# Kernel optimization log

Measured on AMD Instinct MI355X. Metric: run time of the kernel, lower is better.

## Reference

```python
import jax, jax.numpy as jnp
import numpy as np

N_NODES = 50000
N_EDGES = 600000
F_IN = 128
H = 128
NUM_GRAPHS = 64
SELF_LOOP_W = 2.0  # improved=True


def setup_inputs() -> dict:
    key = jax.random.key(0)
    ks = jax.random.split(key, 16)
    x = jax.random.normal(ks[0], (N_NODES, F_IN), dtype=jnp.float32)
    edge_index = jax.random.randint(ks[1], (2, N_EDGES), 0, N_NODES, dtype=jnp.int64)
    batch_index = jnp.sort(jax.random.randint(ks[2], (N_NODES,), 0, NUM_GRAPHS, dtype=jnp.int64))
    edge_weight = jax.random.uniform(ks[3], (N_EDGES,), dtype=jnp.float32)
    def lin(k, fin, fout):
        s = 1.0 / np.sqrt(fin)
        kw, kb = jax.random.split(k)
        W = jax.random.uniform(kw, (fin, fout), minval=-s, maxval=s, dtype=jnp.float32)
        b = jax.random.uniform(kb, (fout,), minval=-s, maxval=s, dtype=jnp.float32)
        return W, b
    W0, b0 = lin(ks[4], F_IN, H)
    W1, b1 = lin(ks[5], H, H)
    W2, b2 = lin(ks[6], H, H)
    W3, b3 = lin(ks[7], H, H)
    Wout, bout = lin(ks[8], 2 * H, 1)
    return dict(x=x, edge_index=edge_index, batch_index=batch_index, edge_weight=edge_weight,
                W0=W0, b0=b0, W1=W1, b1=b1, W2=W2, b2=b2, W3=W3, b3=b3, Wout=Wout, bout=bout)


def reference(x, edge_index, batch_index, edge_weight, W0, b0, W1, b1, W2, b2, W3, b3, Wout, bout):
    N = x.shape[0]
    loop = jnp.arange(N)
    src = jnp.concatenate([edge_index[0], loop])  # [E+N]
    dst = jnp.concatenate([edge_index[1], loop])
    w = jnp.concatenate([edge_weight, jnp.full((N,), SELF_LOOP_W, dtype=x.dtype)])
    # symmetric GCN normalization: deg over destination, norm = d^-1/2[src]*w*d^-1/2[dst]
    deg = jax.ops.segment_sum(w, dst, num_segments=N)
    dinv = jnp.where(deg > 0, jax.lax.rsqrt(deg), 0.0)
    norm = dinv[src] * w * dinv[dst]  # [E+N]

    def conv(h, W, b):
        h = h @ W  # dense transform before aggregation
        msg = h[src] * norm[:, None]
        return jax.ops.segment_sum(msg, dst, num_segments=N) + b

    h = jnp.tanh(conv(x, W0, b0))
    h = jnp.tanh(conv(h, W1, b1))
    h = jnp.tanh(conv(h, W2, b2))
    h = jnp.tanh(conv(h, W3, b3))

    gmax = jax.ops.segment_max(h, batch_index, num_segments=NUM_GRAPHS)
    gmax = jnp.where(jnp.isfinite(gmax), gmax, 0.0)  # guard empty graphs
    cnt = jax.ops.segment_sum(jnp.ones((N,), dtype=h.dtype), batch_index, num_segments=NUM_GRAPHS)
    gmean = jax.ops.segment_sum(h, batch_index, num_segments=NUM_GRAPHS) / jnp.maximum(cnt, 1.0)[:, None]
    hidden = jnp.concatenate([gmax, gmean], axis=1)  # [B, 2H]
    out = hidden @ Wout + bout  # [B, 1]
    return out, hidden
```

## Files before the change

kernel.cpp:

```cpp
#include <hip/hip_runtime.h>
#include <hip/hip_bf16.h>
#include <hip/hip_fp16.h>

typedef __hip_bfloat16 bf16;
typedef _Float16 half8 __attribute__((ext_vector_type(8)));
typedef float f32x4 __attribute__((ext_vector_type(4)));

#define FDIM 128
#define SELF_W 2.0f
#define NGRAPH 64
#define DEG_SCALE 1048576.0f
#define DEG_MASK  ((1ull<<44) - 1ull)

__device__ __forceinline__ float b2f(bf16 v){ return __bfloat162float(v); }

__device__ __forceinline__ float rdf(const void* p, long long i, int f32){
  return f32 ? ((const float*)p)[i] : b2f(((const bf16*)p)[i]);
}
__device__ __forceinline__ int rdi(const void* p, long long i, int i64){
  return i64 ? (int)(((const long long*)p)[i]) : ((const int*)p)[i];
}

__device__ __forceinline__ float tanh_fast(float x){
  float ax = fabsf(x);
  float e  = __expf(-2.0f*ax);
  float r  = (1.0f - e) * __builtin_amdgcn_rcpf(1.0f + e);
  return copysignf(r, x);
}

__global__ __launch_bounds__(256) void k_probe(const unsigned short* __restrict__ x16,
                                               const int* __restrict__ ei32,
                                               int* __restrict__ flags){
  __shared__ int cbig, codd;
  int tid = threadIdx.x;
  if (tid == 0){ cbig = 0; codd = 0; }
  __syncthreads();
  for (int i = tid; i < 4096; i += 256){
    int e = (x16[i] >> 7) & 0xFF;
    if (e >= 134) atomicAdd(&cbig, 1);
  }
  for (int i = tid; i < 512; i += 256){
    if (ei32[2*i + 1] != 0) atomicAdd(&codd, 1);
  }
  __syncthreads();
  if (tid == 0){
    flags[0] = (cbig >= 64) ? 1 : 0;
    flags[1] = (codd < 8)  ? 1 : 0;
  }
}

struct PtrPack { const void* p[10]; };
__global__ __launch_bounds__(256) void k_setup(PtrPack pk, float* __restrict__ pf,
                                               _Float16* __restrict__ wt,
                                               unsigned long long* __restrict__ packed,
                                               const void* __restrict__ bat,
                                               unsigned* __restrict__ gstart,
                                               int N, const int* __restrict__ flags){
  const int sz[10]  = {16384,16384,16384,16384,128,128,128,128,256,1};
  const int dst[10] = {0,16384,32768,49152,65536,65664,65792,65920,66048,66304};
  int i = blockIdx.x*blockDim.x + threadIdx.x;
  if (i < 66305){
    int seg = 0, rem = i;
    while (rem >= sz[seg]){ rem -= sz[seg]; seg++; }
    float v = rdf(pk.p[seg], rem, flags[0]);
    pf[dst[seg] + rem] = v;
    if (seg < 4){
      int k = rem >> 7, n = rem & 127;
      wt[seg*16384 + n*128 + k] = (_Float16)v;
    }
  }
  int stride = gridDim.x*blockDim.x;
  for (int j = i; j < N; j += stride)
    packed[j] = (unsigned long long)(SELF_W * DEG_SCALE);
  if (blockIdx.x == gridDim.x - 1){
    __shared__ unsigned s[NGRAPH+1];
    int g = threadIdx.x;
    int i64 = flags[1];
    if (g <= NGRAPH){
      int lo = 0, hi = N;
      while (lo < hi){ int mid = (lo + hi) >> 1; if (rdi(bat, mid, i64) < g) lo = mid + 1; else hi = mid; }
      s[g] = (unsigned)lo;
    }
    __syncthreads();
    if (g <= NGRAPH) gstart[g] = s[g];
  }
}

__global__ void k_edge_deg(const void* __restrict__ ei, const void* __restrict__ ew,
                           unsigned long long* __restrict__ packed,
                           unsigned* __restrict__ rank,
                           int E, int N, const int* __restrict__ flags){
  int e = blockIdx.x*blockDim.x + threadIdx.x;
  if (e >= E) return;
  int d = rdi(ei, (long long)E + e, flags[1]);
  unsigned r = 0u;
  if ((unsigned)d < (unsigned)N){
    float w = rdf(ew, e, flags[0]);
    unsigned long long add = (1ull << 44) |
        (unsigned long long)__float2uint_rn(w * DEG_SCALE);
    unsigned long long old = atomicAdd(&packed[d], add);
    r = (unsigned)(old >> 44);
  }
  rank[e] = r;
}

__device__ __forceinline__ unsigned wave_incl_scan(unsigned v){
  int lane = threadIdx.x & 63;
  #pragma unroll
  for (int d = 1; d < 64; d <<= 1){
    unsigned t = __shfl_up(v, d, 64);
    if (lane >= d) v += t;
  }
  return v;
}

__global__ __launch_bounds__(256) void k_scan_pre(const unsigned long long* __restrict__ packed,
                                                  float* __restrict__ dinv,
                                                  float* __restrict__ swv,
                                                  unsigned* __restrict__ bsum,
                                                  unsigned* __restrict__ epk, unsigned Epad,
                                                  int N){
  __shared__ unsigned wsh[4];
  int tid = threadIdx.x, lane = tid & 63, wid = tid >> 6;
  unsigned gid = blockIdx.x*blockDim.x + tid, gstr = gridDim.x*blockDim.x;
  for (unsigned j = gid; j < Epad; j += gstr) epk[j] = 0u;
  int i0 = blockIdx.x*1024 + tid*4;
  unsigned tsum = 0u;
  #pragma unroll
  for (int j = 0; j < 4; j++){
    int i = i0 + j;
    if (i < N){
      unsigned long long pv = packed[i];
      tsum += ((unsigned)(pv >> 44) + 7u) & ~7u;
      float d = (float)(pv & DEG_MASK) * (1.0f / DEG_SCALE);
      float di = (d > 0.f) ? rsqrtf(d) : 0.f;
      dinv[i] = di;
      swv[i]  = di * di * SELF_W;
    }
  }
  #pragma unroll
  for (int d = 1; d < 64; d <<= 1) tsum += __shfl_down(tsum, d, 64);
  if (lane == 0) wsh[wid] = tsum;
  __syncthreads();
  if (tid == 0) bsum[blockIdx.x] = wsh[0] + wsh[1] + wsh[2] + wsh[3];
}

__global__ __launch_bounds__(64) void k_scan_mid(unsigned* __restrict__ bsum,
                                                 unsigned* __restrict__ off,
                                                 int nb, int N){
  int lane = threadIdx.x;
  unsigned v = (lane < nb) ? bsum[lane] : 0u;
  unsigned isc = wave_incl_scan(v);
  if (lane < nb) bsum[lane] = isc - v;
  if (lane == 63) off[N] = isc;
}

__global__ __launch_bounds__(256) void k_scan_fin(const unsigned long long* __restrict__ packed,
                                                  const unsigned* __restrict__ bsum,
                                                  unsigned* __restrict__ off, int N){
  __shared__ unsigned wsh[4];
  int tid = threadIdx.x, lane = tid & 63, wid = tid >> 6;
  int i0 = blockIdx.x*1024 + tid*4;
  unsigned v0=0u,v1=0u,v2=0u,v3=0u;
  if (i0+0 < N) v0 = ((unsigned)(packed[i0+0] >> 44) + 7u) & ~7u;
  if (i0+1 < N) v1 = ((unsigned)(packed[i0+1] >> 44) + 7u) & ~7u;
  if (i0+2 < N) v2 = ((unsigned)(packed[i0+2] >> 44) + 7u) & ~7u;
  if (i0+3 < N) v3 = ((unsigned)(packed[i0+3] >> 44) + 7u) & ~7u;
  unsigned tsum = v0+v1+v2+v3;
  unsigned isc = wave_incl_scan(tsum);
  if (lane == 63) wsh[wid] = isc;
  __syncthreads();
  unsigned wbase = 0u;
  #pragma unroll
  for (int w = 0; w < 4; w++) if (w < wid) wbase += wsh[w];
  unsigned ex = bsum[blockIdx.x] + wbase + (isc - tsum);
  if (i0+0 < N) off[i0+0] = ex;
  if (i0+1 < N) off[i0+1] = ex + v0;
  if (i0+2 < N) off[i0+2] = ex + v0 + v1;
  if (i0+3 < N) off[i0+3] = ex + v0 + v1 + v2;
}

__global__ void k_bucket(const void* __restrict__ ei, const void* __restrict__ ew,
                         const float* __restrict__ dinv,
                         const unsigned* __restrict__ off,
                         const unsigned* __restrict__ rank,
                         unsigned* __restrict__ epk,
                         int E, unsigned Epad, int N, const int* __restrict__ flags){
  int e = blockIdx.x*blockDim.x + threadIdx.x;
  if (e >= E) return;
  int s_ = rdi(ei, e, flags[1]);
  int d  = rdi(ei, (long long)E + e, flags[1]);
  if ((unsigned)s_ >= (unsigned)N || (unsigned)d >= (unsigned)N) return;
  unsigned pos = off[d] + rank[e];
  if (pos < Epad){
    float coef = dinv[s_] * rdf(ew, e, flags[0]) * dinv[d];
    _Float16 ch = (_Float16)coef;
    unsigned cu = (unsigned)__builtin_bit_cast(unsigned short, ch);
    epk[pos] = ((unsigned)s_ & 0xffffu) | (cu << 16);
  }
}

template<int MODE>
__global__ __launch_bounds__(256) void k_gemm(const void* __restrict__ in,
                                              const _Float16* __restrict__ WT,
                                              _Float16* __restrict__ outp, int N,
                                              size_t pstride,
                                              const int* __restrict__ flags){
  __shared__ _Float16 sout[4*16*136];
  int tid  = threadIdx.x;
  int wid  = tid >> 6, lane = tid & 63;
  int ln   = lane & 15, quad = lane >> 4;
  int row0 = blockIdx.x * 64;
  int rowA = row0 + wid*16 + ln;
  int rA   = (rowA < N) ? rowA : (N > 0 ? N-1 : 0);

  half8 af[4];
  if (MODE == 1){
    const _Float16* src = (const _Float16*)in;
    #pragma unroll
    for (int kc = 0; kc < 4; kc++)
      af[kc] = *(const half8*)(src + (size_t)kc*pstride + (size_t)rA*32 + quad*8);
  } else {
    if (flags[0]){
      const float* src = (const float*)in + (size_t)rA*FDIM + quad*8;
      #pragma unroll
      for (int kc = 0; kc < 4; kc++){
        float4 a = *(const float4*)(src + kc*32);
        float4 b = *(const float4*)(src + kc*32 + 4);
        half8 h; h[0]=(_Float16)a.x; h[1]=(_Float16)a.y; h[2]=(_Float16)a.z; h[3]=(_Float16)a.w;
        h[4]=(_Float16)b.x; h[5]=(_Float16)b.y; h[6]=(_Float16)b.z; h[7]=(_Float16)b.w;
        af[kc] = h;
      }
    } else {
      const unsigned short* src = (const unsigned short*)in + (size_t)rA*FDIM + quad*8;
      #pragma unroll
      for (int kc = 0; kc < 4; kc++){
        ushort4 u0 = *(const ushort4*)(src + kc*32);
        ushort4 u1 = *(const ushort4*)(src + kc*32 + 4);
        half8 h;
        h[0]=(_Float16)__uint_as_float((unsigned)u0.x<<16);
        h[1]=(_Float16)__uint_as_float((unsigned)u0.y<<16);
        h[2]=(_Float16)__uint_as_float((unsigned)u0.z<<16);
        h[3]=(_Float16)__uint_as_float((unsigned)u0.w<<16);
        h[4]=(_Float16)__uint_as_float((unsigned)u1.x<<16);
        h[5]=(_Float16)__uint_as_float((unsigned)u1.y<<16);
        h[6]=(_Float16)__uint_as_float((unsigned)u1.z<<16);
        h[7]=(_Float16)__uint_as_float((unsigned)u1.w<<16);
        af[kc] = h;
      }
    }
  }

  f32x4 acc[8];
  #pragma unroll
  for (int nt = 0; nt < 8; nt++) acc[nt] = (f32x4){0.f,0.f,0.f,0.f};

  #pragma unroll
  for (int kc = 0; kc < 4; kc++){
    #pragma unroll
    for (int nt = 0; nt < 8; nt++){
      half8 bf = *(const half8*)(WT + (size_t)(nt*16 + ln)*FDIM + kc*32 + quad*8);
      acc[nt] = __builtin_amdgcn_mfma_f32_16x16x32_f16(af[kc], bf, acc[nt], 0, 0, 0);
    }
  }

  _Float16* so = sout + wid*2176;
  #pragma unroll
  for (int nt = 0; nt < 8; nt++)
    #pragma unroll
    for (int reg = 0; reg < 4; reg++)
      so[(quad*4 + reg)*136 + nt*16 + ln] = (_Float16)acc[nt][reg];
  __syncthreads();

  #pragma unroll
  for (int c = 0; c < 4; c++){
    int chunk = tid + c*256;
    int r = chunk >> 4, co = (chunk & 15)*8;
    int row = row0 + r;
    if (row < N){
      half8 v = *(const half8*)(sout + (r>>4)*2176 + (r&15)*136 + co);
      *(half8*)(outp + (size_t)(co>>5)*pstride + (size_t)row*32 + (co & 31)) = v;
    }
  }
}

__global__ __launch_bounds__(256) void k_agg(const _Float16* __restrict__ tp,
                                             const float* __restrict__ swv,
                                             const unsigned* __restrict__ off,
                                             const unsigned* __restrict__ epk,
                                             const float* __restrict__ bias,
                                             _Float16* __restrict__ hp,
                                             int N, size_t pstride){
  int tid  = threadIdx.x;
  int wv   = tid >> 6, lane = tid & 63;
  int quad = lane >> 4, ql = lane & 15;
  int panel = blockIdx.x & 3;
  int n = (blockIdx.x >> 2)*16 + wv*4 + quad;
  bool valid = (n < N);
  int nn = valid ? n : 0;
  const _Float16* tpp = tp + (size_t)panel*pstride;
  const _Float16* myt = tpp + ql*2;

  float sw = swv[nn];
  float2 sv = __half22float2(*(const __half2*)(myt + (size_t)nn*32));
  float a0 = sw * sv.x, a1 = sw * sv.y;
  float b0 = 0.f, b1 = 0.f;

  unsigned beg = off[nn];
  unsigned end = valid ? off[nn+1] : beg;
  for (unsigned i = beg; i < end; i += 8){
    uint4 p0 = *(const uint4*)(epk + i);
    uint4 p1 = *(const uint4*)(epk + i + 4);
    unsigned vs[8] = {p0.x,p0.y,p0.z,p0.w,p1.x,p1.y,p1.z,p1.w};
    __half2 tv[8];
    #pragma unroll
    for (int j = 0; j < 8; j++)
      tv[j] = *(const __half2*)(myt + (size_t)(vs[j] & 0xffffu)*32);
    #pragma unroll
    for (int j = 0; j < 8; j++){
      float w = (float)__builtin_bit_cast(_Float16, (unsigned short)(vs[j] >> 16));
      float2 tf = __half22float2(tv[j]);
      if (j & 1){ b0 += w * tf.x; b1 += w * tf.y; }
      else      { a0 += w * tf.x; a1 += w * tf.y; }
    }
  }
  a0 += b0; a1 += b1;
  int cc = panel*32 + ql*2;
  a0 = tanh_fast(a0 + bias[cc]);
  a1 = tanh_fast(a1 + bias[cc+1]);
  if (valid)
    *(__half2*)(hp + (size_t)panel*pstride + (size_t)n*32 + ql*2) = __floats2half2_rn(a0, a1);
}

__global__ __launch_bounds__(256) void k_pool_part(const _Float16* __restrict__ hp,
                                                   const unsigned* __restrict__ gstart,
                                                   float* __restrict__ pmax,
                                                   float* __restrict__ psum,
                                                   size_t pstride){
  int g = blockIdx.x >> 4, sub = blockIdx.x & 15;
  int tid = threadIdx.x;
  int col = tid & 127, half_ = tid >> 7;
  const _Float16* hpp = hp + (size_t)(col >> 5)*pstride + (col & 31);
  unsigned s0 = gstart[g], s1 = gstart[g+1];
  float m = -INFINITY, sm = 0.f;
  for (unsigned n = s0 + sub*2 + half_; n < s1; n += 32){
    float v = (float)hpp[(size_t)n*32];
    m = fmaxf(m, v); sm += v;
  }
  __shared__ float shm[256], shs[256];
  shm[tid] = m; shs[tid] = sm;
  __syncthreads();
  if (half_ == 0){
    m  = fmaxf(m, shm[tid + 128]);
    sm += shs[tid + 128];
    int slot = (g*16 + sub)*128 + col;
    pmax[slot] = m;
    psum[slot] = sm;
  }
}

__global__ __launch_bounds__(256) void k_pool_out(const float* __restrict__ pmax,
                                                  const float* __restrict__ psum,
                                                  const unsigned* __restrict__ gstart,
                                                  const float* __restrict__ Wout,
                                                  const float* __restrict__ bout,
                                                  void* __restrict__ outp,
                                                  const int* __restrict__ flags){
  int g = blockIdx.x, tid = threadIdx.x;
  int col = tid & 127, sub = tid >> 7;
  unsigned cnt = gstart[g+1] - gstart[g];
  float val;
  if (sub == 0){
    float m = -INFINITY;
    #pragma unroll
    for (int j = 0; j < 16; j++) m = fmaxf(m, pmax[(g*16 + j)*128 + col]);
    val = (cnt > 0 && m > -INFINITY) ? m : 0.f;
  } else {
    float s = 0.f;
    #pragma unroll
    for (int j = 0; j < 16; j++) s += psum[(g*16 + j)*128 + col];
    val = s / (float)(cnt ? cnt : 1u);
  }
  int hcol = sub*128 + col;
  int f32out = flags[0];
  int hidx = NGRAPH + g*(2*FDIM) + hcol;
  if (f32out) ((float*)outp)[hidx] = val;
  else        ((bf16*)outp)[hidx] = __float2bfloat16(val);

  __shared__ float red[256];
  red[hcol] = val * Wout[hcol];
  __syncthreads();
  for (int s = 128; s > 0; s >>= 1){
    if (tid < s) red[tid] += red[tid + s];
    __syncthreads();
  }
  if (tid == 0){
    float o = red[0] + bout[0];
    if (f32out) ((float*)outp)[g] = o;
    else        ((bf16*)outp)[g] = __float2bfloat16(o);
  }
}

extern "C" void kernel_launch(void* const* d_in, const int* in_sizes, int n_in,
                              void* d_out, int out_size, void* d_ws, size_t ws_size,
                              hipStream_t stream){
  int N = in_sizes[0] / FDIM;
  int E = in_sizes[3];
  int NB = (N + 1023) / 1024;
  unsigned Epad = (unsigned)E + 8u*(unsigned)N;
  size_t pstride = (size_t)N * 32;

  char* p = (char*)d_ws;
  auto alloc = [&](size_t bytes){ char* r = p; p += (bytes + 255) & ~(size_t)255; return r; };
  int*       flags  = (int*)      alloc(16);
  float*     pf     = (float*)    alloc((size_t)(66305 + 64)*4);
  _Float16*  wt     = (_Float16*) alloc((size_t)4*FDIM*FDIM*2);
  unsigned long long* packed = (unsigned long long*)alloc((size_t)N*8);
  float*     dinv   = (float*)    alloc((size_t)N*4);
  float*     swv    = (float*)    alloc((size_t)N*4);
  unsigned*  off    = (unsigned*) alloc((size_t)(N+1)*4);
  unsigned*  bsum   = (unsigned*) alloc((size_t)128*4);
  unsigned*  rank   = (unsigned*) alloc((size_t)E*4);
  unsigned*  epk    = (unsigned*) alloc((size_t)Epad*4);
  _Float16*  th     = (_Float16*) alloc((size_t)N*FDIM*2);
  _Float16*  hh     = (_Float16*) alloc((size_t)N*FDIM*2);
  float*     pmax   = (float*)    alloc((size_t)NGRAPH*16*128*4);
  float*     psum   = (float*)    alloc((size_t)NGRAPH*16*128*4);
  unsigned*  gstart = (unsigned*) alloc((size_t)(NGRAPH+1)*4);

  float* bf_[4] = {pf + 65536, pf + 65664, pf + 65792, pf + 65920};
  float* Woutf  = pf + 66048;
  float* boutf  = pf + 66304;

  k_probe<<<1, 256, 0, stream>>>((const unsigned short*)d_in[0], (const int*)d_in[1], flags);

  int gE = (E + 255)/256;
  PtrPack pk;
  pk.p[0]=d_in[4]; pk.p[1]=d_in[6]; pk.p[2]=d_in[8]; pk.p[3]=d_in[10];
  pk.p[4]=d_in[5]; pk.p[5]=d_in[7]; pk.p[6]=d_in[9]; pk.p[7]=d_in[11];
  pk.p[8]=d_in[12]; pk.p[9]=d_in[13];
  k_setup<<<(66305 + 255)/256, 256, 0, stream>>>(pk, pf, wt, packed, d_in[2], gstart, N, flags);
  k_edge_deg<<<gE, 256, 0, stream>>>(d_in[1], d_in[3], packed, rank, E, N, flags);
  k_scan_pre<<<NB, 256, 0, stream>>>(packed, dinv, swv, bsum, epk, Epad, N);
  k_scan_mid<<<1, 64, 0, stream>>>(bsum, off, NB, N);
  k_scan_fin<<<NB, 256, 0, stream>>>(packed, bsum, off, N);
  k_bucket<<<gE, 256, 0, stream>>>(d_in[1], d_in[3], dinv, off, rank, epk, E, Epad, N, flags);

  int gG = (N + 63)/64;
  int gA = ((N + 15)/16)*4;

  k_gemm<0><<<gG, 256, 0, stream>>>(d_in[0], wt + 0*16384, th, N, pstride, flags);
  k_agg<<<gA, 256, 0, stream>>>(th, swv, off, epk, bf_[0], hh, N, pstride);
  for (int l = 1; l < 4; l++){
    k_gemm<1><<<gG, 256, 0, stream>>>(hh, wt + (size_t)l*16384, th, N, pstride, flags);
    k_agg<<<gA, 256, 0, stream>>>(th, swv, off, epk, bf_[l], hh, N, pstride);
  }

  k_pool_part<<<16*NGRAPH, 256, 0, stream>>>(hh, gstart, pmax, psum, pstride);
  k_pool_out<<<NGRAPH, 256, 0, stream>>>(pmax, psum, gstart, Woutf, boutf, d_out, flags);
}
```

Measured before the change: 376.5 us.

## Fuse probe into setup, merge scan mid into fin, 2 edges/thread, prefetch agg

The format probe is folded into every k_setup block, which recomputes the flags redundantly, and the single-block scan_mid is merged into scan_fin, where each block rescans the block sums. Together these remove two tiny kernel launches. The edge degree and bucket kernels now process two edges per thread with half the grid. The aggregation loop prefetches the next group of 8 packed edge entries before gathering, to hide index-load latency. The cost is redundant probe work in each setup block and higher register pressure in the aggregation kernel.

```diff
diff --git a/kernel.cpp b/kernel.cpp
--- a/kernel.cpp
+++ b/kernel.cpp
@@ -26,27 +26,6 @@
   float e  = __expf(-2.0f*ax);
   float r  = (1.0f - e) * __builtin_amdgcn_rcpf(1.0f + e);
   return copysignf(r, x);
-}
-
-__global__ __launch_bounds__(256) void k_probe(const unsigned short* __restrict__ x16,
-                                               const int* __restrict__ ei32,
-                                               int* __restrict__ flags){
-  __shared__ int cbig, codd;
-  int tid = threadIdx.x;
-  if (tid == 0){ cbig = 0; codd = 0; }
-  __syncthreads();
-  for (int i = tid; i < 4096; i += 256){
-    int e = (x16[i] >> 7) & 0xFF;
-    if (e >= 134) atomicAdd(&cbig, 1);
-  }
-  for (int i = tid; i < 512; i += 256){
-    if (ei32[2*i + 1] != 0) atomicAdd(&codd, 1);
-  }
-  __syncthreads();
-  if (tid == 0){
-    flags[0] = (cbig >= 64) ? 1 : 0;
-    flags[1] = (codd < 8)  ? 1 : 0;
-  }
 }
 
 struct PtrPack { const void* p[10]; };
@@ -55,14 +34,37 @@
                                                unsigned long long* __restrict__ packed,
                                                const void* __restrict__ bat,
                                                unsigned* __restrict__ gstart,
-                                               int N, const int* __restrict__ flags){
+                                               const unsigned short* __restrict__ x16,
+                                               const int* __restrict__ ei32,
+                                               int* __restrict__ flags_out,
+                                               int N){
+  __shared__ int cbig, codd, sf32, si64;
+  int tid = threadIdx.x;
+  if (tid == 0){ cbig = 0; codd = 0; }
+  __syncthreads();
+  for (int i = tid; i < 4096; i += 256){
+    int e = (x16[i] >> 7) & 0xFF;
+    if (e >= 134) atomicAdd(&cbig, 1);
+  }
+  for (int i = tid; i < 512; i += 256){
+    if (ei32[2*i + 1] != 0) atomicAdd(&codd, 1);
+  }
+  __syncthreads();
+  if (tid == 0){
+    sf32 = (cbig >= 64) ? 1 : 0;
+    si64 = (codd < 8)  ? 1 : 0;
+    if (blockIdx.x == 0){ flags_out[0] = sf32; flags_out[1] = si64; }
+  }
+  __syncthreads();
+  int f32 = sf32, i64 = si64;
+
   const int sz[10]  = {16384,16384,16384,16384,128,128,128,128,256,1};
   const int dst[10] = {0,16384,32768,49152,65536,65664,65792,65920,66048,66304};
-  int i = blockIdx.x*blockDim.x + threadIdx.x;
+  int i = blockIdx.x*blockDim.x + tid;
   if (i < 66305){
     int seg = 0, rem = i;
     while (rem >= sz[seg]){ rem -= sz[seg]; seg++; }
-    float v = rdf(pk.p[seg], rem, flags[0]);
+    float v = rdf(pk.p[seg], rem, f32);
     pf[dst[seg] + rem] = v;
     if (seg < 4){
       int k = rem >> 7, n = rem & 127;
@@ -74,8 +76,7 @@
     packed[j] = (unsigned long long)(SELF_W * DEG_SCALE);
   if (blockIdx.x == gridDim.x - 1){
     __shared__ unsigned s[NGRAPH+1];
-    int g = threadIdx.x;
-    int i64 = flags[1];
+    int g = tid;
     if (g <= NGRAPH){
       int lo = 0, hi = N;
       while (lo < hi){ int mid = (lo + hi) >> 1; if (rdi(bat, mid, i64) < g) lo = mid + 1; else hi = mid; }
@@ -90,18 +91,28 @@
                            unsigned long long* __restrict__ packed,
                            unsigned* __restrict__ rank,
                            int E, int N, const int* __restrict__ flags){
-  int e = blockIdx.x*blockDim.x + threadIdx.x;
-  if (e >= E) return;
-  int d = rdi(ei, (long long)E + e, flags[1]);
-  unsigned r = 0u;
-  if ((unsigned)d < (unsigned)N){
-    float w = rdf(ew, e, flags[0]);
+  int e0 = 2*(blockIdx.x*blockDim.x + threadIdx.x);
+  if (e0 >= E) return;
+  int i64 = flags[1], f32 = flags[0];
+  int e1 = e0 + 1;
+  bool h1 = (e1 < E);
+  int d0 = rdi(ei, (long long)E + e0, i64);
+  int d1 = h1 ? rdi(ei, (long long)E + e1, i64) : 0;
+  float w0 = rdf(ew, e0, f32);
+  float w1 = h1 ? rdf(ew, e1, f32) : 0.f;
+  unsigned r0 = 0u, r1 = 0u;
+  if ((unsigned)d0 < (unsigned)N){
     unsigned long long add = (1ull << 44) |
-        (unsigned long long)__float2uint_rn(w * DEG_SCALE);
-    unsigned long long old = atomicAdd(&packed[d], add);
-    r = (unsigned)(old >> 44);
-  }
-  rank[e] = r;
+        (unsigned long long)__float2uint_rn(w0 * DEG_SCALE);
+    r0 = (unsigned)(atomicAdd(&packed[d0], add) >> 44);
+  }
+  if (h1 && (unsigned)d1 < (unsigned)N){
+    unsigned long long add = (1ull << 44) |
+        (unsigned long long)__float2uint_rn(w1 * DEG_SCALE);
+    r1 = (unsigned)(atomicAdd(&packed[d1], add) >> 44);
+  }
+  rank[e0] = r0;
+  if (h1) rank[e1] = r1;
 }
 
 __device__ __forceinline__ unsigned wave_incl_scan(unsigned v){
@@ -145,21 +156,19 @@
   if (tid == 0) bsum[blockIdx.x] = wsh[0] + wsh[1] + wsh[2] + wsh[3];
 }
 
-__global__ __launch_bounds__(64) void k_scan_mid(unsigned* __restrict__ bsum,
-                                                 unsigned* __restrict__ off,
-                                                 int nb, int N){
-  int lane = threadIdx.x;
-  unsigned v = (lane < nb) ? bsum[lane] : 0u;
-  unsigned isc = wave_incl_scan(v);
-  if (lane < nb) bsum[lane] = isc - v;
-  if (lane == 63) off[N] = isc;
-}
-
 __global__ __launch_bounds__(256) void k_scan_fin(const unsigned long long* __restrict__ packed,
                                                   const unsigned* __restrict__ bsum,
-                                                  unsigned* __restrict__ off, int N){
+                                                  unsigned* __restrict__ off, int N, int NB){
   __shared__ unsigned wsh[4];
+  __shared__ unsigned sbase, stot;
   int tid = threadIdx.x, lane = tid & 63, wid = tid >> 6;
+  if (tid < 64){
+    unsigned v = (tid < NB) ? bsum[tid] : 0u;
+    unsigned isc = wave_incl_scan(v);
+    if (tid == (int)blockIdx.x) sbase = isc - v;
+    if (tid == 63) stot = isc;
+  }
+  __syncthreads();
   int i0 = blockIdx.x*1024 + tid*4;
   unsigned v0=0u,v1=0u,v2=0u,v3=0u;
   if (i0+0 < N) v0 = ((unsigned)(packed[i0+0] >> 44) + 7u) & ~7u;
@@ -173,11 +182,12 @@
   unsigned wbase = 0u;
   #pragma unroll
   for (int w = 0; w < 4; w++) if (w < wid) wbase += wsh[w];
-  unsigned ex = bsum[blockIdx.x] + wbase + (isc - tsum);
+  unsigned ex = sbase + wbase + (isc - tsum);
   if (i0+0 < N) off[i0+0] = ex;
   if (i0+1 < N) off[i0+1] = ex + v0;
   if (i0+2 < N) off[i0+2] = ex + v0 + v1;
   if (i0+3 < N) off[i0+3] = ex + v0 + v1 + v2;
+  if (blockIdx.x == gridDim.x - 1 && tid == 0) off[N] = stot;
 }
 
 __global__ void k_bucket(const void* __restrict__ ei, const void* __restrict__ ew,
@@ -186,17 +196,23 @@
                          const unsigned* __restrict__ rank,
                          unsigned* __restrict__ epk,
                          int E, unsigned Epad, int N, const int* __restrict__ flags){
-  int e = blockIdx.x*blockDim.x + threadIdx.x;
-  if (e >= E) return;
-  int s_ = rdi(ei, e, flags[1]);
-  int d  = rdi(ei, (long long)E + e, flags[1]);
-  if ((unsigned)s_ >= (unsigned)N || (unsigned)d >= (unsigned)N) return;
-  unsigned pos = off[d] + rank[e];
-  if (pos < Epad){
-    float coef = dinv[s_] * rdf(ew, e, flags[0]) * dinv[d];
-    _Float16 ch = (_Float16)coef;
-    unsigned cu = (unsigned)__builtin_bit_cast(unsigned short, ch);
-    epk[pos] = ((unsigned)s_ & 0xffffu) | (cu << 16);
+  int e0 = 2*(blockIdx.x*blockDim.x + threadIdx.x);
+  if (e0 >= E) return;
+  int i64 = flags[1], f32 = flags[0];
+  #pragma unroll
+  for (int j = 0; j < 2; j++){
+    int e = e0 + j;
+    if (e >= E) break;
+    int s_ = rdi(ei, e, i64);
+    int d  = rdi(ei, (long long)E + e, i64);
+    if ((unsigned)s_ >= (unsigned)N || (unsigned)d >= (unsigned)N) continue;
+    unsigned pos = off[d] + rank[e];
+    if (pos < Epad){
+      float coef = dinv[s_] * rdf(ew, e, f32) * dinv[d];
+      _Float16 ch = (_Float16)coef;
+      unsigned cu = (unsigned)__builtin_bit_cast(unsigned short, ch);
+      epk[pos] = ((unsigned)s_ & 0xffffu) | (cu << 16);
+    }
   }
 }
 
@@ -308,20 +324,27 @@
 
   unsigned beg = off[nn];
   unsigned end = valid ? off[nn+1] : beg;
-  for (unsigned i = beg; i < end; i += 8){
-    uint4 p0 = *(const uint4*)(epk + i);
-    uint4 p1 = *(const uint4*)(epk + i + 4);
-    unsigned vs[8] = {p0.x,p0.y,p0.z,p0.w,p1.x,p1.y,p1.z,p1.w};
-    __half2 tv[8];
-    #pragma unroll
-    for (int j = 0; j < 8; j++)
-      tv[j] = *(const __half2*)(myt + (size_t)(vs[j] & 0xffffu)*32);
-    #pragma unroll
-    for (int j = 0; j < 8; j++){
-      float w = (float)__builtin_bit_cast(_Float16, (unsigned short)(vs[j] >> 16));
-      float2 tf = __half22float2(tv[j]);
-      if (j & 1){ b0 += w * tf.x; b1 += w * tf.y; }
-      else      { a0 += w * tf.x; a1 += w * tf.y; }
+  if (beg < end){
+    uint4 p0 = *(const uint4*)(epk + beg);
+    uint4 p1 = *(const uint4*)(epk + beg + 4);
+    for (unsigned i = beg; i < end; i += 8){
+      unsigned ni  = i + 8;
+      unsigned pre = (ni < end) ? ni : beg;
+      uint4 q0 = *(const uint4*)(epk + pre);
+      uint4 q1 = *(const uint4*)(epk + pre + 4);
+      unsigned vs[8] = {p0.x,p0.y,p0.z,p0.w,p1.x,p1.y,p1.z,p1.w};
+      __half2 tv[8];
+      #pragma unroll
+      for (int j = 0; j < 8; j++)
+        tv[j] = *(const __half2*)(myt + (size_t)(vs[j] & 0xffffu)*32);
+      #pragma unroll
+      for (int j = 0; j < 8; j++){
+        float w = (float)__builtin_bit_cast(_Float16, (unsigned short)(vs[j] >> 16));
+        float2 tf = __half22float2(tv[j]);
+        if (j & 1){ b0 += w * tf.x; b1 += w * tf.y; }
+        else      { a0 += w * tf.x; a1 += w * tf.y; }
+      }
+      p0 = q0; p1 = q1;
     }
   }
   a0 += b0; a1 += b1;
@@ -432,19 +455,18 @@
   float* Woutf  = pf + 66048;
   float* boutf  = pf + 66304;
 
-  k_probe<<<1, 256, 0, stream>>>((const unsigned short*)d_in[0], (const int*)d_in[1], flags);
-
-  int gE = (E + 255)/256;
   PtrPack pk;
   pk.p[0]=d_in[4]; pk.p[1]=d_in[6]; pk.p[2]=d_in[8]; pk.p[3]=d_in[10];
   pk.p[4]=d_in[5]; pk.p[5]=d_in[7]; pk.p[6]=d_in[9]; pk.p[7]=d_in[11];
   pk.p[8]=d_in[12]; pk.p[9]=d_in[13];
-  k_setup<<<(66305 + 255)/256, 256, 0, stream>>>(pk, pf, wt, packed, d_in[2], gstart, N, flags);
-  k_edge_deg<<<gE, 256, 0, stream>>>(d_in[1], d_in[3], packed, rank, E, N, flags);
+  k_setup<<<(66305 + 255)/256, 256, 0, stream>>>(pk, pf, wt, packed, d_in[2], gstart,
+                                                 (const unsigned short*)d_in[0],
+                                                 (const int*)d_in[1], flags, N);
+  int gE2 = (E + 511)/512;
+  k_edge_deg<<<gE2, 256, 0, stream>>>(d_in[1], d_in[3], packed, rank, E, N, flags);
   k_scan_pre<<<NB, 256, 0, stream>>>(packed, dinv, swv, bsum, epk, Epad, N);
-  k_scan_mid<<<1, 64, 0, stream>>>(bsum, off, NB, N);
-  k_scan_fin<<<NB, 256, 0, stream>>>(packed, bsum, off, N);
-  k_bucket<<<gE, 256, 0, stream>>>(d_in[1], d_in[3], dinv, off, rank, epk, E, Epad, N, flags);
+  k_scan_fin<<<NB, 256, 0, stream>>>(packed, bsum, off, N, NB);
+  k_bucket<<<gE2, 256, 0, stream>>>(d_in[1], d_in[3], dinv, off, rank, epk, E, Epad, N, flags);
 
   int gG = (N + 63)/64;
   int gA = ((N + 15)/16)*4;
```

Result: no change. 371.6 us (-1.3%).
